# Performance work log

Hardware: AMD Instinct MI355X
Metric: run time of the kernel (lower is better)

Reference implementation:

```python
import jax, jax.numpy as jnp
import numpy as np

B, T, I, H = 64, 2048, 64, 128


def setup_inputs() -> dict:
    key = jax.random.key(0)
    ks = jax.random.split(key, 6)
    std = 1.0 / np.sqrt(H)
    return {
        "x": jax.random.normal(ks[0], (B, T, I), dtype=jnp.float32),
        "h0": jax.random.normal(ks[1], (B, H), dtype=jnp.float32),
        "W": jax.random.uniform(ks[2], (H, I), dtype=jnp.float32, minval=-std, maxval=std),
        "U": jax.random.uniform(ks[3], (H, H), dtype=jnp.float32, minval=-std, maxval=std),
        "b_ih": jax.random.uniform(ks[4], (H,), dtype=jnp.float32, minval=-std, maxval=std),
        "b_hh": jax.random.uniform(ks[5], (H,), dtype=jnp.float32, minval=-std, maxval=std),
    }


def reference(x, h0, W, U, b_ih, b_hh):
    # Precompute the input projection for all timesteps in one big GEMM:
    # xw[b,t,h] = W x_t + b_ih + b_hh  (biases folded in once)
    xw = jnp.einsum("bti,hi->bth", x, W) + b_ih + b_hh  # [B,T,H]
    xw_t = jnp.swapaxes(xw, 0, 1)  # [T,B,H] for scan over time

    def step(h, xt):
        # vanilla tanh RNN cell: h' = tanh(W x + U h + b_ih + b_hh)
        h_new = jnp.tanh(xt + h @ U.T)
        return h_new, h_new

    h_last, ys = jax.lax.scan(step, h0, xw_t)  # ys: [T,B,H]
    output = jnp.swapaxes(ys, 0, 1)  # batch_first -> [B,T,H]
    return output, h_last
```

## Files before the change

kernel.cpp:

```cpp
#include <hip/hip_runtime.h>


#define RNN_B 64
#define RNN_T 2048
#define RNN_I 64
#define RNN_H 128
#define CH    32
#define NCH   (RNN_T / CH)

__device__ __forceinline__ float fast_tanh(float x) {
  float e = __builtin_amdgcn_exp2f(x * 2.885390081777927f);
  return 1.0f - 2.0f * __builtin_amdgcn_rcpf(e + 1.0f);
}

template <int CTRL>
__device__ __forceinline__ float dpp_add(float s) {
  int o = __builtin_amdgcn_mov_dpp(__float_as_int(s), CTRL, 0xF, 0xF, true);
  return s + __int_as_float(o);
}

__device__ __forceinline__ void fma4(float4& a, const float4 u, const float4 h) {
  a.x = fmaf(u.x, h.x, a.x);
  a.y = fmaf(u.y, h.y, a.y);
  a.z = fmaf(u.z, h.z, a.z);
  a.w = fmaf(u.w, h.w, a.w);
}

__device__ __forceinline__ float hsum(const float4 a) {
  return (a.x + a.y) + (a.z + a.w);
}

__global__ __launch_bounds__(256, 2) void rnn_xw_gemm(
    const float* __restrict__ x, const float* __restrict__ W,
    const float* __restrict__ b_ih, const float* __restrict__ b_hh,
    float* __restrict__ xw) {
  const int tid   = threadIdx.x;
  const int wave  = tid >> 6;
  const int lane  = tid & 63;
  const int whalf = wave & 1;
  const int pair  = wave >> 1;
  const int g2    = lane >> 2;
  const int q2    = lane & 3;

  float4 w[4][4];
#pragma unroll
  for (int r = 0; r < 4; ++r) {
    const float4* Wr =
        (const float4*)(W + (64 * whalf + 4 * g2 + r) * RNN_I + 16 * q2);
#pragma unroll
    for (int m = 0; m < 4; ++m) w[r][m] = Wr[m];
  }
  const int row_own = 64 * whalf + lane;
  const float bias  = b_ih[row_own] + b_hh[row_own];

  __shared__ __align__(16) float4 xs[64 * 16];
  const long rbase = (long)blockIdx.x * 64;
  const float4* xg = (const float4*)(x + rbase * RNN_I);
#pragma unroll
  for (int jj = 0; jj < 4; ++jj) xs[tid + 256 * jj] = xg[tid + 256 * jj];
  __syncthreads();

  for (int i = 0; i < 32; ++i) {
    const int r = 32 * pair + i;
    const float4* xr = xs + r * 16 + q2 * 4;
    float4 a0 = {0,0,0,0}, a1 = {0,0,0,0}, a2 = {0,0,0,0}, a3 = {0,0,0,0};
#pragma unroll
    for (int m = 0; m < 4; ++m) {
      const float4 xv = xr[m];
      fma4(a0, w[0][m], xv);
      fma4(a1, w[1][m], xv);
      fma4(a2, w[2][m], xv);
      fma4(a3, w[3][m], xv);
    }
    float s0 = hsum(a0), s1 = hsum(a1), s2 = hsum(a2), s3 = hsum(a3);
    s0 = dpp_add<0xB1>(s0); s0 = dpp_add<0x4E>(s0);
    s1 = dpp_add<0xB1>(s1); s1 = dpp_add<0x4E>(s1);
    s2 = dpp_add<0xB1>(s2); s2 = dpp_add<0x4E>(s2);
    s3 = dpp_add<0xB1>(s3); s3 = dpp_add<0x4E>(s3);
    const float own = (q2 & 2) ? ((q2 & 1) ? s3 : s2)
                               : ((q2 & 1) ? s1 : s0);
    xw[(rbase + r) * RNN_H + row_own] = own + bias;
  }
}

__global__ __launch_bounds__(256, 1) void rnn_scan(
    const float* xw,
    float* out, float* __restrict__ hlast,
    const float* __restrict__ h0, const float* __restrict__ U) {
  const int b     = blockIdx.x;
  const int tid   = threadIdx.x;
  const int g     = tid >> 3;
  const int j     = tid & 7;
  const int r_own = 4 * g + (j & 3);

  __shared__ __align__(16) float hbuf0[8 * 20];
  __shared__ __align__(16) float hbuf1[8 * 20];
  __shared__ __align__(16) float xbuf[CH * RNN_H];
  __shared__ __align__(16) float obuf[CH * RNN_H];

  float4 u[4][4];
#pragma unroll
  for (int r = 0; r < 4; ++r) {
    const float4* Ur = (const float4*)(U + (4 * g + r) * RNN_H + 16 * j);
#pragma unroll
    for (int m = 0; m < 4; ++m) u[r][m] = Ur[m];
  }

  if (tid < RNN_H)
    hbuf0[(tid >> 4) * 20 + (tid & 15)] = h0[b * RNN_H + tid];

  const int hoff = (r_own >> 4) * 20 + (r_own & 15);
  const long base   = (long)b * RNN_T * RNN_H;
  const float4* xw4 = (const float4*)(xw + base);
  float4* out4      = (float4*)(out + base);
  float4* xb4       = (float4*)xbuf;
  const float4* ob4 = (const float4*)obuf;

  auto step = [&](const float* src, float* dst, int tc) {
    const float xv = xbuf[tc * RNN_H + r_own];
    const float4* hp = (const float4*)(src + 20 * j);
    float4 a0 = {0,0,0,0}, a1 = {0,0,0,0}, a2 = {0,0,0,0}, a3 = {0,0,0,0};
#pragma unroll
    for (int m = 0; m < 4; ++m) {
      const float4 hv = hp[m];
      fma4(a0, u[0][m], hv);
      fma4(a1, u[1][m], hv);
      fma4(a2, u[2][m], hv);
      fma4(a3, u[3][m], hv);
    }
    float s0 = hsum(a0), s1 = hsum(a1), s2 = hsum(a2), s3 = hsum(a3);
    s0 = dpp_add<0xB1>(s0); s0 = dpp_add<0x4E>(s0); s0 = dpp_add<0x141>(s0);
    s1 = dpp_add<0xB1>(s1); s1 = dpp_add<0x4E>(s1); s1 = dpp_add<0x141>(s1);
    s2 = dpp_add<0xB1>(s2); s2 = dpp_add<0x4E>(s2); s2 = dpp_add<0x141>(s2);
    s3 = dpp_add<0xB1>(s3); s3 = dpp_add<0x4E>(s3); s3 = dpp_add<0x141>(s3);
    const float own = (j & 2) ? ((j & 1) ? s3 : s2)
                              : ((j & 1) ? s1 : s0);
    const float val = fast_tanh(own + xv);
    float* wp = (j < 4) ? (dst + hoff) : (obuf + tc * RNN_H + r_own);
    *wp = val;
    __syncthreads();
  };

  for (int c = 0; c < NCH; ++c) {
#pragma unroll
    for (int jj = 0; jj < 4; ++jj)
      xb4[tid + 256 * jj] = xw4[(long)c * 1024 + tid + 256 * jj];
    if (c > 0) {
#pragma unroll
      for (int jj = 0; jj < 4; ++jj)
        out4[(long)(c - 1) * 1024 + tid + 256 * jj] = ob4[tid + 256 * jj];
    }
    __syncthreads();

    for (int tc = 0; tc < CH; tc += 2) {
      step(hbuf0, hbuf1, tc);
      step(hbuf1, hbuf0, tc + 1);
    }
  }

#pragma unroll
  for (int jj = 0; jj < 4; ++jj)
    out4[(long)(NCH - 1) * 1024 + tid + 256 * jj] = ob4[tid + 256 * jj];
  if (tid < RNN_H)
    hlast[b * RNN_H + tid] = hbuf0[(tid >> 4) * 20 + (tid & 15)];
}

extern "C" void kernel_launch(void* const* d_in, const int* in_sizes, int n_in,
                              void* d_out, int out_size, void* d_ws, size_t ws_size,
                              hipStream_t stream) {
  const float* x    = (const float*)d_in[0];
  const float* h0   = (const float*)d_in[1];
  const float* W    = (const float*)d_in[2];
  const float* U    = (const float*)d_in[3];
  const float* b_ih = (const float*)d_in[4];
  const float* b_hh = (const float*)d_in[5];

  float* out   = (float*)d_out;
  float* hlast = out + (long)RNN_B * RNN_T * RNN_H;

  rnn_xw_gemm<<<(RNN_B * RNN_T) / 64, 256, 0, stream>>>(x, W, b_ih, b_hh, out);
  rnn_scan<<<RNN_B, 256, 0, stream>>>(out, out, hlast, h0, U);
}
```

Baseline: 759.6 us.

## Prefetch next xw chunk into registers and write outputs directly to global

```diff
diff --git a/kernel.cpp b/kernel.cpp
--- a/kernel.cpp
+++ b/kernel.cpp
@@ -30,6 +30,10 @@
   return (a.x + a.y) + (a.z + a.w);
 }
 
+__device__ __forceinline__ void pin4(float4& v) {
+  asm volatile("" : "+v"(v.x), "+v"(v.y), "+v"(v.z), "+v"(v.w));
+}
+
 __global__ __launch_bounds__(256, 2) void rnn_xw_gemm(
     const float* __restrict__ x, const float* __restrict__ W,
     const float* __restrict__ b_ih, const float* __restrict__ b_hh,
@@ -48,7 +52,7 @@
     const float4* Wr =
         (const float4*)(W + (64 * whalf + 4 * g2 + r) * RNN_I + 16 * q2);
 #pragma unroll
-    for (int m = 0; m < 4; ++m) w[r][m] = Wr[m];
+    for (int m = 0; m < 4; ++m) { w[r][m] = Wr[m]; pin4(w[r][m]); }
   }
   const int row_own = 64 * whalf + lane;
   const float bias  = b_ih[row_own] + b_hh[row_own];
@@ -96,14 +100,13 @@
   __shared__ __align__(16) float hbuf0[8 * 20];
   __shared__ __align__(16) float hbuf1[8 * 20];
   __shared__ __align__(16) float xbuf[CH * RNN_H];
-  __shared__ __align__(16) float obuf[CH * RNN_H];
 
   float4 u[4][4];
 #pragma unroll
   for (int r = 0; r < 4; ++r) {
     const float4* Ur = (const float4*)(U + (4 * g + r) * RNN_H + 16 * j);
 #pragma unroll
-    for (int m = 0; m < 4; ++m) u[r][m] = Ur[m];
+    for (int m = 0; m < 4; ++m) { u[r][m] = Ur[m]; pin4(u[r][m]); }
   }
 
   if (tid < RNN_H)
@@ -112,11 +115,13 @@
   const int hoff = (r_own >> 4) * 20 + (r_own & 15);
   const long base   = (long)b * RNN_T * RNN_H;
   const float4* xw4 = (const float4*)(xw + base);
-  float4* out4      = (float4*)(out + base);
+  float* outp       = out + base;
   float4* xb4       = (float4*)xbuf;
-  const float4* ob4 = (const float4*)obuf;
 
-  auto step = [&](const float* src, float* dst, int tc) {
+  float4 p0 = xw4[tid], p1 = xw4[tid + 256],
+         p2 = xw4[tid + 512], p3 = xw4[tid + 768];
+
+  auto step = [&](const float* src, float* dst, int tc, float* ob) {
     const float xv = xbuf[tc * RNN_H + r_own];
     const float4* hp = (const float4*)(src + 20 * j);
     float4 a0 = {0,0,0,0}, a1 = {0,0,0,0}, a2 = {0,0,0,0}, a3 = {0,0,0,0};
@@ -136,31 +141,31 @@
     const float own = (j & 2) ? ((j & 1) ? s3 : s2)
                               : ((j & 1) ? s1 : s0);
     const float val = fast_tanh(own + xv);
-    float* wp = (j < 4) ? (dst + hoff) : (obuf + tc * RNN_H + r_own);
-    *wp = val;
+    if (j < 4) {
+      dst[hoff] = val;
+    } else {
+      ob[tc * RNN_H + r_own] = val;
+    }
     __syncthreads();
   };
 
   for (int c = 0; c < NCH; ++c) {
-#pragma unroll
-    for (int jj = 0; jj < 4; ++jj)
-      xb4[tid + 256 * jj] = xw4[(long)c * 1024 + tid + 256 * jj];
-    if (c > 0) {
-#pragma unroll
-      for (int jj = 0; jj < 4; ++jj)
-        out4[(long)(c - 1) * 1024 + tid + 256 * jj] = ob4[tid + 256 * jj];
+    xb4[tid] = p0; xb4[tid + 256] = p1;
+    xb4[tid + 512] = p2; xb4[tid + 768] = p3;
+    if (c + 1 < NCH) {
+      const float4* nx = xw4 + (long)(c + 1) * 1024;
+      p0 = nx[tid]; p1 = nx[tid + 256];
+      p2 = nx[tid + 512]; p3 = nx[tid + 768];
     }
     __syncthreads();
 
+    float* ob = outp + (long)c * CH * RNN_H;
     for (int tc = 0; tc < CH; tc += 2) {
-      step(hbuf0, hbuf1, tc);
-      step(hbuf1, hbuf0, tc + 1);
+      step(hbuf0, hbuf1, tc, ob);
+      step(hbuf1, hbuf0, tc + 1, ob);
     }
   }
 
-#pragma unroll
-  for (int jj = 0; jj < 4; ++jj)
-    out4[(long)(NCH - 1) * 1024 + tid + 256 * jj] = ob4[tid + 256 * jj];
   if (tid < RNN_H)
     hlast[b * RNN_H + tid] = hbuf0[(tid >> 4) * 20 + (tid & 15)];
 }
```

New measurement: 879.5 us. +15.8%, slower.
